# Optimization experiments

Measured on AMD Instinct MI355X. Metric: run time of the kernel, lower is better.

## Reference

```python
import jax, jax.numpy as jnp
import numpy as np

B, L, D = 4, 2048, 768          # batch, seq_len, model dim
DI, DS, DTR, DCONV = 1536, 16, 48, 4  # d_inner, d_state, dt_rank, d_conv


def setup_inputs() -> dict:
    key = jax.random.key(0)
    ks = jax.random.split(key, 8)
    s = 0.02
    f32 = jnp.float32
    return {
        "x": jax.random.normal(ks[0], (B, L, D), f32),
        "ln_w": jnp.ones((D,), f32),
        "ln_b": jnp.zeros((D,), f32),
        "W_in": (jax.random.normal(ks[1], (D, 2 * DI), f32) * s),
        "conv_w": (jax.random.normal(ks[2], (DI, DCONV), f32) * s),
        "conv_b": jnp.zeros((DI,), f32),
        "W_x": (jax.random.normal(ks[3], (DI, DTR + 2 * DS), f32) * s),
        "W_dt": (jax.random.normal(ks[4], (DTR, DI), f32) * s),
        "b_dt": jnp.full((DI,), -4.6, f32),  # softplus(b_dt) ~ 0.01 init dt
        "A_log": jnp.log(jnp.tile(jnp.arange(1.0, DS + 1.0, dtype=f32), (DI, 1))),
        "D_param": jnp.ones((DI,), f32),
        "W_out": (jax.random.normal(ks[5], (DI, D), f32) * s),
    }


def reference(x, ln_w, ln_b, W_in, conv_w, conv_b, W_x, W_dt, b_dt,
              A_log, D_param, W_out):
    eps = 1e-5

    def layernorm(h):
        mu = h.mean(-1, keepdims=True)
        var = ((h - mu) ** 2).mean(-1, keepdims=True)
        return (h - mu) * jax.lax.rsqrt(var + eps) * ln_w + ln_b

    A = -jnp.exp(A_log)  # [DI, DS]

    def mixer(h):
        # h: [B, L, D]
        xz = h @ W_in                       # [B, L, 2*DI]
        u, z = jnp.split(xz, 2, axis=-1)    # each [B, L, DI]
        # causal depthwise conv1d (kernel DCONV)
        pad = jnp.pad(u, ((0, 0), (DCONV - 1, 0), (0, 0)))
        conv = conv_b
        for k in range(DCONV):
            conv = conv + pad[:, k:k + L, :] * conv_w[:, k]
        u = jax.nn.silu(conv)               # [B, L, DI]
        xdb = u @ W_x                       # [B, L, DTR+2*DS]
        dt_raw = xdb[..., :DTR]
        Bm = xdb[..., DTR:DTR + DS]         # [B, L, DS]
        Cm = xdb[..., DTR + DS:]            # [B, L, DS]
        dt = jax.nn.softplus(dt_raw @ W_dt + b_dt)  # [B, L, DI]

        def step(hst, inp):
            dt_t, B_t, C_t, u_t = inp       # [B,DI],[B,DS],[B,DS],[B,DI]
            dA = jnp.exp(dt_t[..., None] * A)              # [B,DI,DS]
            hst = hst * dA + (dt_t * u_t)[..., None] * B_t[:, None, :]
            y = jnp.einsum('bds,bs->bd', hst, C_t)
            return hst, y

        h0 = jnp.zeros((h.shape[0], DI, DS), u.dtype)
        xs = (jnp.swapaxes(dt, 0, 1), jnp.swapaxes(Bm, 0, 1),
              jnp.swapaxes(Cm, 0, 1), jnp.swapaxes(u, 0, 1))
        _, ys = jax.lax.scan(step, h0, xs)  # ys: [L, B, DI]
        y = jnp.swapaxes(ys, 0, 1) + u * D_param
        y = y * jax.nn.silu(z)
        return y @ W_out                    # [B, L, D]

    xn = layernorm(x)
    x_fwd = mixer(xn)
    x_bwd = jnp.flip(mixer(jnp.flip(xn, 1)), 1)
    return x + 0.5 * (x_fwd + x_bwd)
```

## Files before the change

kernel.cpp:

```cpp
#include <hip/hip_runtime.h>
#include <hip/hip_bf16.h>

#define B_  4
#define L_  2048
#define D_  768
#define DI_ 1536
#define DS_ 16
#define DTR_ 48
#define ROWS_ (B_*L_)

typedef __hip_bfloat16 bf16;
typedef __attribute__((ext_vector_type(8))) short bf16x8;
typedef __attribute__((ext_vector_type(4))) float f32x4;

__device__ __forceinline__ float silu_f(float x) { return x / (1.f + __expf(-x)); }
__device__ __forceinline__ float softplus_f(float x) { return x > 15.f ? x : __logf(1.f + __expf(x)); }
__device__ __forceinline__ float b2f(bf16 v) { return __bfloat162float(v); }
__device__ __forceinline__ bf16 f2b(float v) { return __float2bfloat16(v); }
__device__ __forceinline__ float bfb(unsigned short u) {
    union { unsigned int i; float f; } w; w.i = ((unsigned int)u) << 16; return w.f;
}
__device__ __forceinline__ short f2bbits(float v) {
    bf16 t = __float2bfloat16(v);
    return *(short*)&t;
}
__device__ __forceinline__ void gload_lds16(const void* g, void* l) {
    __builtin_amdgcn_global_load_lds((const __attribute__((address_space(1))) void*)g,
                                     (__attribute__((address_space(3))) void*)l, 16, 0, 0);
}

__global__ __launch_bounds__(256) void convert_wt(const float* __restrict__ W,
                                                  bf16* __restrict__ Wt,
                                                  int K, int N) {
    __shared__ float tile[32][33];
    int bx = blockIdx.x * 32;
    int by = blockIdx.y * 32;
    int tx = threadIdx.x & 31, ty = threadIdx.x >> 5;
#pragma unroll
    for (int i = 0; i < 32; i += 8)
        tile[ty + i][tx] = W[(size_t)(by + ty + i) * N + bx + tx];
    __syncthreads();
#pragma unroll
    for (int i = 0; i < 32; i += 8)
        Wt[(size_t)(bx + ty + i) * K + by + tx] = f2b(tile[tx][ty + i]);
}

__global__ __launch_bounds__(256) void convert_wxt(const float* __restrict__ W,
                                                   bf16* __restrict__ Wt) {
    int idx = blockIdx.x * 256 + threadIdx.x;
    int n = idx / DI_, k = idx % DI_;
    Wt[idx] = f2b(W[(size_t)k * 80 + n]);
}

__global__ __launch_bounds__(256) void convert_wdt(const float* __restrict__ W,
                                                   bf16* __restrict__ Wt) {
    int idx = blockIdx.x * 256 + threadIdx.x;
    int n = idx >> 6, k = idx & 63;
    Wt[idx] = f2b(k < DTR_ ? W[(size_t)k * DI_ + n] : 0.f);
}

__global__ __launch_bounds__(256) void ln_kernel(const float* __restrict__ x,
                                                 const float* __restrict__ w,
                                                 const float* __restrict__ b,
                                                 bf16* __restrict__ xn) {
    int row = blockIdx.x;
    const float* xr = x + (size_t)row * D_;
    bf16* on = xn + (size_t)row * D_;
    int t = threadIdx.x;
    float v[3];
    float s1 = 0.f, s2 = 0.f;
#pragma unroll
    for (int i = 0; i < 3; i++) { v[i] = xr[t + 256 * i]; s1 += v[i]; s2 += v[i] * v[i]; }
#pragma unroll
    for (int off = 32; off > 0; off >>= 1) { s1 += __shfl_down(s1, off); s2 += __shfl_down(s2, off); }
    __shared__ float sa[4], sb[4];
    int wid = t >> 6, lane = t & 63;
    if (lane == 0) { sa[wid] = s1; sb[wid] = s2; }
    __syncthreads();
    if (t == 0) { sa[0] = sa[0] + sa[1] + sa[2] + sa[3]; sb[0] = sb[0] + sb[1] + sb[2] + sb[3]; }
    __syncthreads();
    float mu = sa[0] * (1.f / D_);
    float var = sb[0] * (1.f / D_) - mu * mu;
    float rs = rsqrtf(var + 1e-5f);
#pragma unroll
    for (int i = 0; i < 3; i++) {
        int c = t + 256 * i;
        on[c] = f2b((v[i] - mu) * rs * w[c] + b[c]);
    }
}

__global__ __launch_bounds__(256) void gemm_in_mfma(const bf16* __restrict__ A,
                                                    const bf16* __restrict__ Bt,
                                                    bf16* __restrict__ u_pre,
                                                    bf16* __restrict__ z_s) {
    const int K = D_;
    __shared__ __align__(16) short As[128 * 32];
    __shared__ __align__(16) short Bs[128 * 32];
    int tid = threadIdx.x;
    int lane = tid & 63, wid = tid >> 6;
    int wr = wid >> 1, wc = wid & 1;
    int m0 = blockIdx.y * 128, n0 = blockIdx.x * 128;
    f32x4 acc[4][4];
#pragma unroll
    for (int i = 0; i < 4; i++)
#pragma unroll
        for (int j = 0; j < 4; j++) acc[i][j] = (f32x4){0.f, 0.f, 0.f, 0.f};

    int rl = lane & 15;
    int kb = (lane >> 4) * 8;

    for (int k0 = 0; k0 < K; k0 += 32) {
#pragma unroll
        for (int c = 0; c < 2; c++) {
            int s = c * 256 + tid;
            int r = s >> 2, sg = (s & 3) * 8;
            gload_lds16(A + (size_t)(m0 + r) * K + k0 + sg, &As[(c * 256 + wid * 64) * 8]);
            gload_lds16(Bt + (size_t)(n0 + r) * K + k0 + sg, &Bs[(c * 256 + wid * 64) * 8]);
        }
        __syncthreads();
        bf16x8 av[4], bv[4];
#pragma unroll
        for (int i = 0; i < 4; i++)
            av[i] = *(const bf16x8*)&As[(wr * 64 + i * 16 + rl) * 32 + kb];
#pragma unroll
        for (int j = 0; j < 4; j++)
            bv[j] = *(const bf16x8*)&Bs[(wc * 64 + j * 16 + rl) * 32 + kb];
#pragma unroll
        for (int i = 0; i < 4; i++)
#pragma unroll
            for (int j = 0; j < 4; j++)
                acc[i][j] = __builtin_amdgcn_mfma_f32_16x16x32_bf16(av[i], bv[j], acc[i][j], 0, 0, 0);
        __syncthreads();
    }
#pragma unroll
    for (int i = 0; i < 4; i++) {
        int mrow = m0 + wr * 64 + i * 16 + (lane >> 4) * 4;
#pragma unroll
        for (int j = 0; j < 4; j++) {
            int ncol = n0 + wc * 64 + j * 16 + rl;
#pragma unroll
            for (int r = 0; r < 4; r++) {
                float v = acc[i][j][r];
                int m = mrow + r;
                if (ncol < DI_) u_pre[(size_t)m * DI_ + ncol] = f2b(v);
                else            z_s[(size_t)m * DI_ + (ncol - DI_)] = f2b(silu_f(v));
            }
        }
    }
}

__global__ __launch_bounds__(256) void gemm_out_mfma(const bf16* __restrict__ gf,
                                                     const bf16* __restrict__ gb,
                                                     const bf16* __restrict__ Bt,
                                                     const float* __restrict__ resid,
                                                     float* __restrict__ C) {
    const int K = DI_, N = D_;
    __shared__ __align__(16) short As[128 * 32];
    __shared__ __align__(16) short Bs[128 * 32];
    int tid = threadIdx.x;
    int lane = tid & 63, wid = tid >> 6;
    int wr = wid >> 1, wc = wid & 1;
    int m0 = blockIdx.y * 128, n0 = blockIdx.x * 128;
    f32x4 acc[4][4];
#pragma unroll
    for (int i = 0; i < 4; i++)
#pragma unroll
        for (int j = 0; j < 4; j++) acc[i][j] = (f32x4){0.f, 0.f, 0.f, 0.f};

    int rl = lane & 15;
    int kb = (lane >> 4) * 8;

    for (int k0 = 0; k0 < K; k0 += 32) {
#pragma unroll
        for (int c = 0; c < 2; c++) {
            int s = c * 256 + tid;
            int r = s >> 2, sg = (s & 3) * 8;
            size_t off = (size_t)(m0 + r) * K + k0 + sg;
            const unsigned short* pf = (const unsigned short*)(gf + off);
            const unsigned short* pb = (const unsigned short*)(gb + off);
            ushort4 a0 = *(const ushort4*)pf, a1 = *(const ushort4*)(pf + 4);
            ushort4 b0 = *(const ushort4*)pb, b1 = *(const ushort4*)(pb + 4);
            bf16x8 st;
            st[0] = f2bbits(bfb(a0.x) + bfb(b0.x));
            st[1] = f2bbits(bfb(a0.y) + bfb(b0.y));
            st[2] = f2bbits(bfb(a0.z) + bfb(b0.z));
            st[3] = f2bbits(bfb(a0.w) + bfb(b0.w));
            st[4] = f2bbits(bfb(a1.x) + bfb(b1.x));
            st[5] = f2bbits(bfb(a1.y) + bfb(b1.y));
            st[6] = f2bbits(bfb(a1.z) + bfb(b1.z));
            st[7] = f2bbits(bfb(a1.w) + bfb(b1.w));
            *(bf16x8*)&As[s * 8] = st;
            gload_lds16(Bt + (size_t)(n0 + r) * K + k0 + sg, &Bs[(c * 256 + wid * 64) * 8]);
        }
        __syncthreads();
        bf16x8 av[4], bv[4];
#pragma unroll
        for (int i = 0; i < 4; i++)
            av[i] = *(const bf16x8*)&As[(wr * 64 + i * 16 + rl) * 32 + kb];
#pragma unroll
        for (int j = 0; j < 4; j++)
            bv[j] = *(const bf16x8*)&Bs[(wc * 64 + j * 16 + rl) * 32 + kb];
#pragma unroll
        for (int i = 0; i < 4; i++)
#pragma unroll
            for (int j = 0; j < 4; j++)
                acc[i][j] = __builtin_amdgcn_mfma_f32_16x16x32_bf16(av[i], bv[j], acc[i][j], 0, 0, 0);
        __syncthreads();
    }
#pragma unroll
    for (int i = 0; i < 4; i++) {
        int mrow = m0 + wr * 64 + i * 16 + (lane >> 4) * 4;
#pragma unroll
        for (int j = 0; j < 4; j++) {
            int ncol = n0 + wc * 64 + j * 16 + rl;
#pragma unroll
            for (int r = 0; r < 4; r++) {
                size_t idx = (size_t)(mrow + r) * N + ncol;
                C[idx] = resid[idx] + 0.5f * acc[i][j][r];
            }
        }
    }
}

__global__ __launch_bounds__(256) void conv_kernel8(const bf16* __restrict__ up,
                                                    const float* __restrict__ cw,
                                                    const float* __restrict__ cb,
                                                    bf16* __restrict__ uf,
                                                    bf16* __restrict__ ub) {
    const int dpb = DI_ / 8;
    int idx = blockIdx.x * 256 + threadIdx.x;
    int d8 = (idx % dpb) * 8;
    int bl = idx / dpb;
    int l = bl % L_, b = bl / L_;
    const bf16* base = up + (size_t)b * L_ * DI_ + d8;
    float um[7][8];
#pragma unroll
    for (int k = 0; k < 7; k++) {
        int ll = l - 3 + k;
        if (ll >= 0 && ll < L_) {
            bf16x8 v = *(const bf16x8*)(base + (size_t)ll * DI_);
#pragma unroll
            for (int e = 0; e < 8; e++) um[k][e] = bfb((unsigned short)v[e]);
        } else {
#pragma unroll
            for (int e = 0; e < 8; e++) um[k][e] = 0.f;
        }
    }
    bf16x8 of, ob;
#pragma unroll
    for (int e = 0; e < 8; e++) {
        float4 w = *(const float4*)(cw + (size_t)(d8 + e) * 4);
        float bias = cb[d8 + e];
        float cf  = bias + um[0][e] * w.x + um[1][e] * w.y + um[2][e] * w.z + um[3][e] * w.w;
        float cbw = bias + um[6][e] * w.x + um[5][e] * w.y + um[4][e] * w.z + um[3][e] * w.w;
        of[e] = f2bbits(silu_f(cf));
        ob[e] = f2bbits(silu_f(cbw));
    }
    size_t oidx = (size_t)bl * DI_ + d8;
    *(bf16x8*)(uf + oidx) = of;
    *(bf16x8*)(ub + oidx) = ob;
}

__global__ __launch_bounds__(256) void xdb_mfma(const bf16* __restrict__ uf,
                                                const bf16* __restrict__ ub,
                                                const bf16* __restrict__ Wxt,
                                                float* __restrict__ xf,
                                                float* __restrict__ xb,
                                                bf16* __restrict__ drf,
                                                bf16* __restrict__ drb) {
    const bf16* u = blockIdx.y ? ub : uf;
    float* xout = blockIdx.y ? xb : xf;
    bf16* dout = blockIdx.y ? drb : drf;
    int m0 = blockIdx.x * 64;
    __shared__ __align__(16) short As[64 * 64];
    int tid = threadIdx.x;
    int lane = tid & 63, wid = tid >> 6;
    int rl = lane & 15, hi = lane >> 4;
    f32x4 acc[5];
#pragma unroll
    for (int j = 0; j < 5; j++) acc[j] = (f32x4){0.f, 0.f, 0.f, 0.f};

    int r_loc = wid * 16 + rl;

    for (int k0 = 0; k0 < DI_; k0 += 64) {
#pragma unroll
        for (int t = 0; t < 2; t++) {
            int s = t * 256 + tid;
            int row = s >> 3, c = s & 7;
            int cs = c ^ (row & 7);
            gload_lds16(u + (size_t)(m0 + row) * DI_ + k0 + cs * 8,
                        &As[(t * 256 + wid * 64) * 8]);
        }
        __syncthreads();
        bf16x8 av[2];
#pragma unroll
        for (int kc = 0; kc < 2; kc++) {
            int c = kc * 4 + hi;
            av[kc] = *(const bf16x8*)&As[r_loc * 64 + ((c ^ (r_loc & 7)) * 8)];
        }
#pragma unroll
        for (int j = 0; j < 5; j++)
#pragma unroll
            for (int kc = 0; kc < 2; kc++) {
                bf16x8 bv = *(const bf16x8*)(Wxt + (size_t)(j * 16 + rl) * DI_ + k0 + kc * 32 + hi * 8);
                acc[j] = __builtin_amdgcn_mfma_f32_16x16x32_bf16(av[kc], bv, acc[j], 0, 0, 0);
            }
        __syncthreads();
    }
#pragma unroll
    for (int j = 0; j < 5; j++) {
        int col = j * 16 + rl;
#pragma unroll
        for (int r = 0; r < 4; r++) {
            int m = m0 + wid * 16 + hi * 4 + r;
            float v = acc[j][r];
            if (col >= DTR_) xout[(size_t)m * 80 + col] = v;
            if (col < DTR_)      dout[(size_t)m * 64 + col] = f2b(v);
            else if (col < 64)   dout[(size_t)m * 64 + col] = f2b(0.f);
        }
    }
}

__global__ __launch_bounds__(256) void gemm_dt_mfma(const bf16* __restrict__ drf,
                                                    const bf16* __restrict__ drb,
                                                    const bf16* __restrict__ Wdt_t,
                                                    const float* __restrict__ bdt,
                                                    bf16* __restrict__ dtf,
                                                    bf16* __restrict__ dtb) {
    const bf16* A = blockIdx.z ? drb : drf;
    bf16* out = blockIdx.z ? dtb : dtf;
    int m0 = blockIdx.y * 64;
    int n0 = blockIdx.x * 256;
    __shared__ __align__(16) short As[64 * 64];
    int tid = threadIdx.x, lane = tid & 63, wid = tid >> 6;
    int rl = lane & 15, hi = lane >> 4;
#pragma unroll
    for (int t = 0; t < 2; t++) {
        int s = t * 256 + tid;
        int row = s >> 3, c = s & 7;
        gload_lds16(A + (size_t)(m0 + row) * 64 + (c ^ (row & 7)) * 8,
                    &As[(t * 256 + wid * 64) * 8]);
    }
    __syncthreads();
    int r_loc = wid * 16 + rl;
    bf16x8 av[2];
#pragma unroll
    for (int kc = 0; kc < 2; kc++) {
        int c = kc * 4 + hi;
        av[kc] = *(const bf16x8*)&As[r_loc * 64 + ((c ^ (r_loc & 7)) * 8)];
    }
    f32x4 acc[16];
#pragma unroll
    for (int j = 0; j < 16; j++) acc[j] = (f32x4){0.f, 0.f, 0.f, 0.f};
#pragma unroll
    for (int j = 0; j < 16; j++)
#pragma unroll
        for (int kc = 0; kc < 2; kc++) {
            bf16x8 bv = *(const bf16x8*)(Wdt_t + (size_t)(n0 + j * 16 + rl) * 64 + kc * 32 + hi * 8);
            acc[j] = __builtin_amdgcn_mfma_f32_16x16x32_bf16(av[kc], bv, acc[j], 0, 0, 0);
        }
#pragma unroll
    for (int j = 0; j < 16; j++) {
        int n = n0 + j * 16 + rl;
        float bb = bdt[n];
#pragma unroll
        for (int r = 0; r < 4; r++) {
            int m = m0 + wid * 16 + hi * 4 + r;
            out[(size_t)m * DI_ + n] = f2b(softplus_f(acc[j][r] + bb));
        }
    }
}

__global__ __launch_bounds__(256) void scan_part1(const bf16* __restrict__ dtf,
                                                  const bf16* __restrict__ dtb,
                                                  const bf16* __restrict__ uff,
                                                  const bf16* __restrict__ ubb,
                                                  const float* __restrict__ xdbf,
                                                  const float* __restrict__ xdbb,
                                                  const float* __restrict__ A_log,
                                                  float* __restrict__ Pbuf,
                                                  float* __restrict__ Ebuf,
                                                  int NC, int CL) {
    int dir = blockIdx.z;
    int b = blockIdx.y / NC, c = blockIdx.y % NC;
    int d = blockIdx.x * 256 + threadIdx.x;
    size_t cbase = (size_t)b * L_ * DI_ + d;
    const bf16* dt = (dir ? dtb : dtf) + cbase;
    const bf16* uu = (dir ? ubb : uff) + cbase;
    const float* xdb = (dir ? xdbb : xdbf) + (size_t)b * L_ * 80;

    float a[DS_];
    int fast = 1;
#pragma unroll
    for (int s = 0; s < DS_; s++) {
        a[s] = -__expf(A_log[d * DS_ + s]);
        fast = fast && (fabsf(a[s] + (float)(s + 1)) < 1e-4f * (s + 1));
    }
    fast = __syncthreads_and(fast);

    float h[DS_], P[DS_];
#pragma unroll
    for (int s = 0; s < DS_; s++) { h[s] = 0.f; P[s] = 1.f; }

    __shared__ float Bsh[32][DS_];
    int li = threadIdx.x >> 3, ci = (threadIdx.x & 7) * 4;

    for (int t0 = 0; t0 < CL; t0 += 32) {
        __syncthreads();
        {
            int tt = c * CL + t0 + li;
            int l = dir ? (L_ - 1 - tt) : tt;
            if (ci < 16) {
                float4 v = *(const float4*)(xdb + (size_t)l * 80 + DTR_ + ci);
                Bsh[li][ci + 0] = v.x; Bsh[li][ci + 1] = v.y;
                Bsh[li][ci + 2] = v.z; Bsh[li][ci + 3] = v.w;
            }
        }
        __syncthreads();
        for (int q = 0; q < 32; q++) {
            int tt = c * CL + t0 + q;
            int l = dir ? (L_ - 1 - tt) : tt;
            size_t off = (size_t)l * DI_;
            float dtv = b2f(dt[off]);
            float uv = b2f(uu[off]);
            float xu = dtv * uv;
            float dAv[DS_];
            if (fast) {
                float r = __expf(-dtv);
                float p = 1.f;
#pragma unroll
                for (int s = 0; s < DS_; s++) { p *= r; dAv[s] = p; }
            } else {
#pragma unroll
                for (int s = 0; s < DS_; s++) dAv[s] = __expf(dtv * a[s]);
            }
#pragma unroll
            for (int s = 0; s < DS_; s++) {
                h[s] = h[s] * dAv[s] + xu * Bsh[q][s];
                P[s] *= dAv[s];
            }
        }
    }
    size_t base = (((size_t)(dir * B_ + b) * NC + c) * DS_) * DI_ + d;
#pragma unroll
    for (int s = 0; s < DS_; s++) {
        Pbuf[base + (size_t)s * DI_] = P[s];
        Ebuf[base + (size_t)s * DI_] = h[s];
    }
}

__global__ __launch_bounds__(256) void scan_part2(const float* __restrict__ Pbuf,
                                                  float* __restrict__ Ebuf,
                                                  int NC) {
    int idx = blockIdx.x * 256 + threadIdx.x;
    int d = idx % DI_;
    int rest = idx / DI_;
    int s = rest % DS_;
    int bb = rest / DS_;
    size_t base = ((size_t)bb * NC * DS_ + s) * DI_ + d;
    float H = 0.f;
    for (int c = 0; c < NC; c++) {
        size_t aa = base + (size_t)c * DS_ * DI_;
        float P = Pbuf[aa], E = Ebuf[aa];
        Ebuf[aa] = H;
        H = P * H + E;
    }
}

__global__ __launch_bounds__(256) void scan_part3(const bf16* __restrict__ dtf,
                                                  const bf16* __restrict__ dtb,
                                                  const bf16* __restrict__ uff,
                                                  const bf16* __restrict__ ubb,
                                                  const float* __restrict__ xdbf,
                                                  const float* __restrict__ xdbb,
                                                  const bf16* __restrict__ z_s,
                                                  const float* __restrict__ A_log,
                                                  const float* __restrict__ Dp_,
                                                  const float* __restrict__ Ebuf,
                                                  bf16* __restrict__ gf,
                                                  bf16* __restrict__ gb,
                                                  int NC, int CL) {
    int dir = blockIdx.z;
    int b = blockIdx.y / NC, c = blockIdx.y % NC;
    int d = blockIdx.x * 256 + threadIdx.x;
    size_t cbase = (size_t)b * L_ * DI_ + d;
    const bf16* dt = (dir ? dtb : dtf) + cbase;
    const bf16* uu = (dir ? ubb : uff) + cbase;
    const float* xdb = (dir ? xdbb : xdbf) + (size_t)b * L_ * 80;
    const bf16* zp = z_s + cbase;
    bf16* g = (dir ? gb : gf) + cbase;

    float a[DS_];
    int fast = 1;
#pragma unroll
    for (int s = 0; s < DS_; s++) {
        a[s] = -__expf(A_log[d * DS_ + s]);
        fast = fast && (fabsf(a[s] + (float)(s + 1)) < 1e-4f * (s + 1));
    }
    fast = __syncthreads_and(fast);
    float Dp = Dp_[d];

    float h[DS_];
    size_t base = (((size_t)(dir * B_ + b) * NC + c) * DS_) * DI_ + d;
#pragma unroll
    for (int s = 0; s < DS_; s++) h[s] = Ebuf[base + (size_t)s * DI_];

    __shared__ float Bsh[32][DS_];
    __shared__ float Csh[32][DS_];
    int li = threadIdx.x >> 3, ci = (threadIdx.x & 7) * 4;

    for (int t0 = 0; t0 < CL; t0 += 32) {
        __syncthreads();
        {
            int tt = c * CL + t0 + li;
            int l = dir ? (L_ - 1 - tt) : tt;
            float4 v = *(const float4*)(xdb + (size_t)l * 80 + DTR_ + ci);
            if (ci < 16) {
                Bsh[li][ci + 0] = v.x; Bsh[li][ci + 1] = v.y;
                Bsh[li][ci + 2] = v.z; Bsh[li][ci + 3] = v.w;
            } else {
                Csh[li][ci - 16] = v.x; Csh[li][ci - 15] = v.y;
                Csh[li][ci - 14] = v.z; Csh[li][ci - 13] = v.w;
            }
        }
        __syncthreads();
        for (int q = 0; q < 32; q++) {
            int tt = c * CL + t0 + q;
            int l = dir ? (L_ - 1 - tt) : tt;
            size_t off = (size_t)l * DI_;
            float dtv = b2f(dt[off]);
            float uv = b2f(uu[off]);
            float zv = b2f(zp[off]);
            float xu = dtv * uv;
            float dAv[DS_];
            if (fast) {
                float r = __expf(-dtv);
                float p = 1.f;
#pragma unroll
                for (int s = 0; s < DS_; s++) { p *= r; dAv[s] = p; }
            } else {
#pragma unroll
                for (int s = 0; s < DS_; s++) dAv[s] = __expf(dtv * a[s]);
            }
            float y = 0.f;
#pragma unroll
            for (int s = 0; s < DS_; s++) {
                h[s] = h[s] * dAv[s] + xu * Bsh[q][s];
                y += h[s] * Csh[q][s];
            }
            g[off] = f2b((y + uv * Dp) * zv);
        }
    }
}

__global__ __launch_bounds__(256) void scan_kernel(const bf16* __restrict__ dtf,
                                                   const bf16* __restrict__ dtb,
                                                   const bf16* __restrict__ uff,
                                                   const bf16* __restrict__ ubb,
                                                   const float* __restrict__ xdbf,
                                                   const float* __restrict__ xdbb,
                                                   const bf16* __restrict__ z_s,
                                                   const float* __restrict__ A_log,
                                                   const float* __restrict__ Dp_,
                                                   bf16* __restrict__ gf,
                                                   bf16* __restrict__ gb) {
    int dir = blockIdx.z;
    int b = blockIdx.y;
    int d = blockIdx.x * 256 + threadIdx.x;
    size_t cbase = (size_t)b * L_ * DI_ + d;
    const bf16* dt = (dir ? dtb : dtf) + cbase;
    const bf16* uu = (dir ? ubb : uff) + cbase;
    const float* xdb = (dir ? xdbb : xdbf) + (size_t)b * L_ * 80;
    const bf16* zp = z_s + cbase;
    bf16* g = (dir ? gb : gf) + cbase;
    float a[DS_];
#pragma unroll
    for (int s = 0; s < DS_; s++) a[s] = -__expf(A_log[d * DS_ + s]);
    float Dp = Dp_[d];
    float h[DS_];
#pragma unroll
    for (int s = 0; s < DS_; s++) h[s] = 0.f;
    __shared__ float Bsh[32][16];
    __shared__ float Csh[32][16];
    int li = threadIdx.x >> 3, ci = (threadIdx.x & 7) * 4;
    for (int t0 = 0; t0 < L_; t0 += 32) {
        __syncthreads();
        {
            int tt = t0 + li;
            int l = dir ? (L_ - 1 - tt) : tt;
            float4 v = *(const float4*)(xdb + (size_t)l * 80 + DTR_ + ci);
            if (ci < 16) {
                Bsh[li][ci + 0] = v.x; Bsh[li][ci + 1] = v.y; Bsh[li][ci + 2] = v.z; Bsh[li][ci + 3] = v.w;
            } else {
                Csh[li][ci - 16] = v.x; Csh[li][ci - 15] = v.y; Csh[li][ci - 14] = v.z; Csh[li][ci - 13] = v.w;
            }
        }
        __syncthreads();
        for (int q = 0; q < 32; q++) {
            int tstep = t0 + q;
            int l = dir ? (L_ - 1 - tstep) : tstep;
            size_t off = (size_t)l * DI_;
            float dtv = b2f(dt[off]);
            float uv = b2f(uu[off]);
            float zv = b2f(zp[off]);
            float xu = dtv * uv;
            float y = 0.f;
#pragma unroll
            for (int s = 0; s < DS_; s++) {
                float dA = __expf(dtv * a[s]);
                h[s] = h[s] * dA + xu * Bsh[q][s];
                y += h[s] * Csh[q][s];
            }
            g[off] = f2b((y + uv * Dp) * zv);
        }
    }
}

extern "C" void kernel_launch(void* const* d_in, const int* in_sizes, int n_in,
                              void* d_out, int out_size, void* d_ws, size_t ws_size,
                              hipStream_t stream) {
    const float* x      = (const float*)d_in[0];
    const float* ln_w   = (const float*)d_in[1];
    const float* ln_b   = (const float*)d_in[2];
    const float* W_in   = (const float*)d_in[3];
    const float* conv_w = (const float*)d_in[4];
    const float* conv_b = (const float*)d_in[5];
    const float* W_x    = (const float*)d_in[6];
    const float* W_dt   = (const float*)d_in[7];
    const float* b_dt   = (const float*)d_in[8];
    const float* A_log  = (const float*)d_in[9];
    const float* D_par  = (const float*)d_in[10];
    const float* W_out  = (const float*)d_in[11];
    float* out = (float*)d_out;

    const size_t NBbf = (size_t)ROWS_ * DI_ * sizeof(bf16);
    const size_t XDB4 = (size_t)ROWS_ * 80 * sizeof(float);
    const size_t WT1  = (size_t)D_ * 2 * DI_ * sizeof(bf16);
    const size_t WT2  = (size_t)DI_ * D_ * sizeof(bf16);
    const size_t WXT  = (size_t)80 * DI_ * sizeof(bf16);
    const size_t WDT  = (size_t)DI_ * 64 * sizeof(bf16);
    const size_t DR   = (size_t)ROWS_ * 64 * sizeof(bf16);
    const size_t BASE = 7 * NBbf + 2 * XDB4 + WT1 + WT2 + WXT + WDT + 2 * DR;
    if (ws_size < BASE) return;

    auto pe_bytes = [&](int NC) { return (size_t)2 * B_ * NC * DS_ * DI_ * sizeof(float); };
    int NC = 0;
    if (ws_size >= BASE + 2 * pe_bytes(32)) NC = 32;
    else if (ws_size >= BASE + 2 * pe_bytes(16)) NC = 16;
    const int CL = NC ? L_ / NC : 0;

    char* p = (char*)d_ws;
    bf16* z_s   = (bf16*)p;  p += NBbf;
    bf16* u_f   = (bf16*)p;  p += NBbf;
    bf16* u_b   = (bf16*)p;  p += NBbf;
    bf16* slotA = (bf16*)p;  p += NBbf;
    bf16* dt_b  = (bf16*)p;  p += NBbf;
    char* slotB = p;         p += NBbf;
    bf16* g_b   = (bf16*)p;  p += NBbf;
    float* xdb_f = (float*)p; p += XDB4;
    float* xdb_b = (float*)p; p += XDB4;
    bf16* Wt_in  = (bf16*)p;  p += WT1;
    bf16* Wt_out = (bf16*)p;  p += WT2;
    bf16* Wxt    = (bf16*)p;  p += WXT;
    bf16* Wdt_t  = (bf16*)p;  p += WDT;
    bf16* dr_f   = (bf16*)p;  p += DR;
    bf16* dr_b   = (bf16*)p;  p += DR;
    float* Pbuf = (float*)p;  p += NC ? pe_bytes(NC) : 0;
    float* Ebuf = (float*)p;

    bf16* u_pre = slotA;
    bf16* dt_f  = slotA;
    bf16* xn    = (bf16*)slotB;
    bf16* g_f   = (bf16*)slotB;

    convert_wt<<<dim3((2 * DI_) / 32, D_ / 32), 256, 0, stream>>>(W_in, Wt_in, D_, 2 * DI_);
    convert_wt<<<dim3(D_ / 32, DI_ / 32), 256, 0, stream>>>(W_out, Wt_out, DI_, D_);
    convert_wxt<<<(80 * DI_) / 256, 256, 0, stream>>>(W_x, Wxt);
    convert_wdt<<<(DI_ * 64) / 256, 256, 0, stream>>>(W_dt, Wdt_t);
    ln_kernel<<<ROWS_, 256, 0, stream>>>(x, ln_w, ln_b, xn);
    gemm_in_mfma<<<dim3((2 * DI_) / 128, ROWS_ / 128), 256, 0, stream>>>(xn, Wt_in, u_pre, z_s);
    conv_kernel8<<<(ROWS_ * DI_ / 8) / 256, 256, 0, stream>>>(u_pre, conv_w, conv_b, u_f, u_b);
    xdb_mfma<<<dim3(ROWS_ / 64, 2), 256, 0, stream>>>(u_f, u_b, Wxt, xdb_f, xdb_b, dr_f, dr_b);
    gemm_dt_mfma<<<dim3(DI_ / 256, ROWS_ / 64, 2), 256, 0, stream>>>(dr_f, dr_b, Wdt_t, b_dt, dt_f, dt_b);
    if (NC) {
        scan_part1<<<dim3(DI_ / 256, B_ * NC, 2), 256, 0, stream>>>(
            dt_f, dt_b, u_f, u_b, xdb_f, xdb_b, A_log, Pbuf, Ebuf, NC, CL);
        scan_part2<<<(2 * B_ * DS_ * DI_) / 256, 256, 0, stream>>>(Pbuf, Ebuf, NC);
        scan_part3<<<dim3(DI_ / 256, B_ * NC, 2), 256, 0, stream>>>(
            dt_f, dt_b, u_f, u_b, xdb_f, xdb_b, z_s, A_log, D_par, Ebuf, g_f, g_b, NC, CL);
    } else {
        scan_kernel<<<dim3(DI_ / 256, B_, 2), 256, 0, stream>>>(
            dt_f, dt_b, u_f, u_b, xdb_f, xdb_b, z_s, A_log, D_par, g_f, g_b);
    }
    gemm_out_mfma<<<dim3(D_ / 128, ROWS_ / 128), 256, 0, stream>>>(g_f, g_b, Wt_out, x, out);
}
```

Measured before the change: 445.9 us.

## Read B/C directly from global in scans, swizzle GEMM block order

The chunked scan kernels stop staging B and C through shared memory with block barriers. Each thread now loads B and C straight from global memory as uniform vector loads, which should hit cache. The first scan pass also computes the chunk decay product from the summed dt instead of multiplying it step by step. Both GEMMs remap block indices with a stride-8 swizzle to change the order tiles are scheduled across XCDs/L2. This trades LDS traffic and syncs for redundant cached global loads per thread, and gives slightly different rounding in the decay product.

Result: faster. 416.4 us (-6.6%).

```diff
diff --git a/kernel.cpp b/kernel.cpp
--- a/kernel.cpp
+++ b/kernel.cpp
@@ -94,12 +94,16 @@
                                                     bf16* __restrict__ u_pre,
                                                     bf16* __restrict__ z_s) {
     const int K = D_;
+    constexpr int NX = (2 * DI_) / 128;
+    constexpr int NWG = NX * (ROWS_ / 128);
     __shared__ __align__(16) short As[128 * 32];
     __shared__ __align__(16) short Bs[128 * 32];
     int tid = threadIdx.x;
     int lane = tid & 63, wid = tid >> 6;
     int wr = wid >> 1, wc = wid & 1;
-    int m0 = blockIdx.y * 128, n0 = blockIdx.x * 128;
+    int bid = blockIdx.y * NX + blockIdx.x;
+    bid = (bid & 7) * (NWG / 8) + (bid >> 3);
+    int m0 = (bid / NX) * 128, n0 = (bid % NX) * 128;
     f32x4 acc[4][4];
 #pragma unroll
     for (int i = 0; i < 4; i++)
@@ -155,12 +159,16 @@
                                                      const float* __restrict__ resid,
                                                      float* __restrict__ C) {
     const int K = DI_, N = D_;
+    constexpr int NX = D_ / 128;
+    constexpr int NWG = NX * (ROWS_ / 128);
     __shared__ __align__(16) short As[128 * 32];
     __shared__ __align__(16) short Bs[128 * 32];
     int tid = threadIdx.x;
     int lane = tid & 63, wid = tid >> 6;
     int wr = wid >> 1, wc = wid & 1;
-    int m0 = blockIdx.y * 128, n0 = blockIdx.x * 128;
+    int bid = blockIdx.y * NX + blockIdx.x;
+    bid = (bid & 7) * (NWG / 8) + (bid >> 3);
+    int m0 = (bid / NX) * 128, n0 = (bid % NX) * 128;
     f32x4 acc[4][4];
 #pragma unroll
     for (int i = 0; i < 4; i++)
@@ -400,44 +408,55 @@
 
     float h[DS_], P[DS_];
 #pragma unroll
-    for (int s = 0; s < DS_; s++) { h[s] = 0.f; P[s] = 1.f; }
-
-    __shared__ float Bsh[32][DS_];
-    int li = threadIdx.x >> 3, ci = (threadIdx.x & 7) * 4;
-
-    for (int t0 = 0; t0 < CL; t0 += 32) {
-        __syncthreads();
-        {
-            int tt = c * CL + t0 + li;
-            int l = dir ? (L_ - 1 - tt) : tt;
-            if (ci < 16) {
-                float4 v = *(const float4*)(xdb + (size_t)l * 80 + DTR_ + ci);
-                Bsh[li][ci + 0] = v.x; Bsh[li][ci + 1] = v.y;
-                Bsh[li][ci + 2] = v.z; Bsh[li][ci + 3] = v.w;
-            }
-        }
-        __syncthreads();
-        for (int q = 0; q < 32; q++) {
-            int tt = c * CL + t0 + q;
+    for (int s = 0; s < DS_; s++) h[s] = 0.f;
+
+    int t0 = c * CL;
+    if (fast) {
+        float sdt = 0.f;
+        for (int tt = t0; tt < t0 + CL; ++tt) {
             int l = dir ? (L_ - 1 - tt) : tt;
             size_t off = (size_t)l * DI_;
             float dtv = b2f(dt[off]);
             float uv = b2f(uu[off]);
             float xu = dtv * uv;
-            float dAv[DS_];
-            if (fast) {
-                float r = __expf(-dtv);
-                float p = 1.f;
-#pragma unroll
-                for (int s = 0; s < DS_; s++) { p *= r; dAv[s] = p; }
-            } else {
-#pragma unroll
-                for (int s = 0; s < DS_; s++) dAv[s] = __expf(dtv * a[s]);
-            }
+            sdt += dtv;
+            float r = __expf(-dtv);
+            const float* br = xdb + (size_t)l * 80 + DTR_;
+            float4 b0 = *(const float4*)(br);
+            float4 b1 = *(const float4*)(br + 4);
+            float4 b2 = *(const float4*)(br + 8);
+            float4 b3 = *(const float4*)(br + 12);
+            float Bv[16] = {b0.x, b0.y, b0.z, b0.w, b1.x, b1.y, b1.z, b1.w,
+                            b2.x, b2.y, b2.z, b2.w, b3.x, b3.y, b3.z, b3.w};
+            float p = 1.f;
+#pragma unroll
+            for (int s = 0; s < DS_; s++) { p *= r; h[s] = h[s] * p + xu * Bv[s]; }
+        }
+        float Rc = __expf(-sdt);
+        float p = 1.f;
+#pragma unroll
+        for (int s = 0; s < DS_; s++) { p *= Rc; P[s] = p; }
+    } else {
+#pragma unroll
+        for (int s = 0; s < DS_; s++) P[s] = 1.f;
+        for (int tt = t0; tt < t0 + CL; ++tt) {
+            int l = dir ? (L_ - 1 - tt) : tt;
+            size_t off = (size_t)l * DI_;
+            float dtv = b2f(dt[off]);
+            float uv = b2f(uu[off]);
+            float xu = dtv * uv;
+            const float* br = xdb + (size_t)l * 80 + DTR_;
+            float4 b0 = *(const float4*)(br);
+            float4 b1 = *(const float4*)(br + 4);
+            float4 b2 = *(const float4*)(br + 8);
+            float4 b3 = *(const float4*)(br + 12);
+            float Bv[16] = {b0.x, b0.y, b0.z, b0.w, b1.x, b1.y, b1.z, b1.w,
+                            b2.x, b2.y, b2.z, b2.w, b3.x, b3.y, b3.z, b3.w};
 #pragma unroll
             for (int s = 0; s < DS_; s++) {
-                h[s] = h[s] * dAv[s] + xu * Bsh[q][s];
-                P[s] *= dAv[s];
+                float dA = __expf(dtv * a[s]);
+                h[s] = h[s] * dA + xu * Bv[s];
+                P[s] *= dA;
             }
         }
     }
@@ -505,48 +524,65 @@
 #pragma unroll
     for (int s = 0; s < DS_; s++) h[s] = Ebuf[base + (size_t)s * DI_];
 
-    __shared__ float Bsh[32][DS_];
-    __shared__ float Csh[32][DS_];
-    int li = threadIdx.x >> 3, ci = (threadIdx.x & 7) * 4;
-
-    for (int t0 = 0; t0 < CL; t0 += 32) {
-        __syncthreads();
-        {
-            int tt = c * CL + t0 + li;
-            int l = dir ? (L_ - 1 - tt) : tt;
-            float4 v = *(const float4*)(xdb + (size_t)l * 80 + DTR_ + ci);
-            if (ci < 16) {
-                Bsh[li][ci + 0] = v.x; Bsh[li][ci + 1] = v.y;
-                Bsh[li][ci + 2] = v.z; Bsh[li][ci + 3] = v.w;
-            } else {
-                Csh[li][ci - 16] = v.x; Csh[li][ci - 15] = v.y;
-                Csh[li][ci - 14] = v.z; Csh[li][ci - 13] = v.w;
-            }
-        }
-        __syncthreads();
-        for (int q = 0; q < 32; q++) {
-            int tt = c * CL + t0 + q;
+    int t0 = c * CL;
+    if (fast) {
+        for (int tt = t0; tt < t0 + CL; ++tt) {
             int l = dir ? (L_ - 1 - tt) : tt;
             size_t off = (size_t)l * DI_;
             float dtv = b2f(dt[off]);
             float uv = b2f(uu[off]);
             float zv = b2f(zp[off]);
             float xu = dtv * uv;
-            float dAv[DS_];
-            if (fast) {
-                float r = __expf(-dtv);
-                float p = 1.f;
-#pragma unroll
-                for (int s = 0; s < DS_; s++) { p *= r; dAv[s] = p; }
-            } else {
-#pragma unroll
-                for (int s = 0; s < DS_; s++) dAv[s] = __expf(dtv * a[s]);
+            float r = __expf(-dtv);
+            const float* br = xdb + (size_t)l * 80 + DTR_;
+            float4 b0 = *(const float4*)(br);
+            float4 b1 = *(const float4*)(br + 4);
+            float4 b2 = *(const float4*)(br + 8);
+            float4 b3 = *(const float4*)(br + 12);
+            float4 c0 = *(const float4*)(br + 16);
+            float4 c1 = *(const float4*)(br + 20);
+            float4 c2 = *(const float4*)(br + 24);
+            float4 c3 = *(const float4*)(br + 28);
+            float Bv[16] = {b0.x, b0.y, b0.z, b0.w, b1.x, b1.y, b1.z, b1.w,
+                            b2.x, b2.y, b2.z, b2.w, b3.x, b3.y, b3.z, b3.w};
+            float Cv[16] = {c0.x, c0.y, c0.z, c0.w, c1.x, c1.y, c1.z, c1.w,
+                            c2.x, c2.y, c2.z, c2.w, c3.x, c3.y, c3.z, c3.w};
+            float p = 1.f, y = 0.f;
+#pragma unroll
+            for (int s = 0; s < DS_; s++) {
+                p *= r;
+                h[s] = h[s] * p + xu * Bv[s];
+                y += h[s] * Cv[s];
             }
+            g[off] = f2b((y + uv * Dp) * zv);
+        }
+    } else {
+        for (int tt = t0; tt < t0 + CL; ++tt) {
+            int l = dir ? (L_ - 1 - tt) : tt;
+            size_t off = (size_t)l * DI_;
+            float dtv = b2f(dt[off]);
+            float uv = b2f(uu[off]);
+            float zv = b2f(zp[off]);
+            float xu = dtv * uv;
+            const float* br = xdb + (size_t)l * 80 + DTR_;
+            float4 b0 = *(const float4*)(br);
+            float4 b1 = *(const float4*)(br + 4);
+            float4 b2 = *(const float4*)(br + 8);
+            float4 b3 = *(const float4*)(br + 12);
+            float4 c0 = *(const float4*)(br + 16);
+            float4 c1 = *(const float4*)(br + 20);
+            float4 c2 = *(const float4*)(br + 24);
+            float4 c3 = *(const float4*)(br + 28);
+            float Bv[16] = {b0.x, b0.y, b0.z, b0.w, b1.x, b1.y, b1.z, b1.w,
+                            b2.x, b2.y, b2.z, b2.w, b3.x, b3.y, b3.z, b3.w};
+            float Cv[16] = {c0.x, c0.y, c0.z, c0.w, c1.x, c1.y, c1.z, c1.w,
+                            c2.x, c2.y, c2.z, c2.w, c3.x, c3.y, c3.z, c3.w};
             float y = 0.f;
 #pragma unroll
             for (int s = 0; s < DS_; s++) {
-                h[s] = h[s] * dAv[s] + xu * Bsh[q][s];
-                y += h[s] * Csh[q][s];
+                float dA = __expf(dtv * a[s]);
+                h[s] = h[s] * dA + xu * Bv[s];
+                y += h[s] * Cv[s];
             }
             g[off] = f2b((y + uv * Dp) * zv);
         }
@@ -580,39 +616,22 @@
     float h[DS_];
 #pragma unroll
     for (int s = 0; s < DS_; s++) h[s] = 0.f;
-    __shared__ float Bsh[32][16];
-    __shared__ float Csh[32][16];
-    int li = threadIdx.x >> 3, ci = (threadIdx.x & 7) * 4;
-    for (int t0 = 0; t0 < L_; t0 += 32) {
-        __syncthreads();
-        {
-            int tt = t0 + li;
-            int l = dir ? (L_ - 1 - tt) : tt;
-            float4 v = *(const float4*)(xdb + (size_t)l * 80 + DTR_ + ci);
-            if (ci < 16) {
-                Bsh[li][ci + 0] = v.x; Bsh[li][ci + 1] = v.y; Bsh[li][ci + 2] = v.z; Bsh[li][ci + 3] = v.w;
-            } else {
-                Csh[li][ci - 16] = v.x; Csh[li][ci - 15] = v.y; Csh[li][ci - 14] = v.z; Csh[li][ci - 13] = v.w;
-            }
-        }
-        __syncthreads();
-        for (int q = 0; q < 32; q++) {
-            int tstep = t0 + q;
-            int l = dir ? (L_ - 1 - tstep) : tstep;
-            size_t off = (size_t)l * DI_;
-            float dtv = b2f(dt[off]);
-            float uv = b2f(uu[off]);
-            float zv = b2f(zp[off]);
-            float xu = dtv * uv;
-            float y = 0.f;
-#pragma unroll
-            for (int s = 0; s < DS_; s++) {
-                float dA = __expf(dtv * a[s]);
-                h[s] = h[s] * dA + xu * Bsh[q][s];
-                y += h[s] * Csh[q][s];
-            }
-            g[off] = f2b((y + uv * Dp) * zv);
-        }
+    for (int tt = 0; tt < L_; ++tt) {
+        int l = dir ? (L_ - 1 - tt) : tt;
+        size_t off = (size_t)l * DI_;
+        float dtv = b2f(dt[off]);
+        float uv = b2f(uu[off]);
+        float zv = b2f(zp[off]);
+        float xu = dtv * uv;
+        const float* br = xdb + (size_t)l * 80 + DTR_;
+        float y = 0.f;
+#pragma unroll
+        for (int s = 0; s < DS_; s++) {
+            float dA = __expf(dtv * a[s]);
+            h[s] = h[s] * dA + xu * br[s];
+            y += h[s] * br[16 + s];
+        }
+        g[off] = f2b((y + uv * Dp) * zv);
     }
 }
 
```
